# Optimization experiments

Hardware: AMD Instinct MI355X
Metric: run time of the kernel (lower is better)

## Reference

```python
import jax, jax.numpy as jnp
import numpy as np

N_GRAPHS = 8192
NODES_PER_GRAPH = 62
IN_CH = 4
HID = 64
NUM_CLASSES = 3
DEG = 8
N = N_GRAPHS * NODES_PER_GRAPH        # 507904 total nodes
E = N * DEG                            # 4063232 edges
BN_EPS = 1e-5


def setup_inputs() -> dict:
    key = jax.random.key(0)
    ks = jax.random.split(key, 24)

    def lin_w(k, i, o):
        return (jax.random.normal(k, (i, o), jnp.float32) / np.float32(np.sqrt(i)))

    inp = {
        "x": jax.random.normal(ks[0], (N, IN_CH), jnp.float32),
        "edge_src": jax.random.randint(ks[1], (E,), 0, N, dtype=jnp.int32),
        "edge_dst": jax.random.randint(ks[2], (E,), 0, N, dtype=jnp.int32),
        "num_graphs": N_GRAPHS,
        # conv1 MLP: Linear(4,64) -> ReLU -> Linear(64,64)
        "W1a": lin_w(ks[3], IN_CH, HID), "b1a": jnp.zeros((HID,), jnp.float32),
        "W1b": lin_w(ks[4], HID, HID),   "b1b": jnp.zeros((HID,), jnp.float32),
        "g1": jnp.ones((HID,), jnp.float32), "be1": jnp.zeros((HID,), jnp.float32),
        # conv2 MLP
        "W2a": lin_w(ks[5], HID, HID), "b2a": jnp.zeros((HID,), jnp.float32),
        "W2b": lin_w(ks[6], HID, HID), "b2b": jnp.zeros((HID,), jnp.float32),
        "g2": jnp.ones((HID,), jnp.float32), "be2": jnp.zeros((HID,), jnp.float32),
        # conv3 MLP
        "W3a": lin_w(ks[7], HID, HID), "b3a": jnp.zeros((HID,), jnp.float32),
        "W3b": lin_w(ks[8], HID, HID), "b3b": jnp.zeros((HID,), jnp.float32),
        "g3": jnp.ones((HID,), jnp.float32), "be3": jnp.zeros((HID,), jnp.float32),
        # final classifier fc2 (fc1 is unused in the original forward)
        "Wfc": lin_w(ks[9], HID, NUM_CLASSES), "bfc": jnp.zeros((NUM_CLASSES,), jnp.float32),
    }
    return inp


def _gin_conv(x, src, dst, Wa, ba, Wb, bb):
    # GINConv with eps=0: mlp(x_i + sum_{j->i} x_j)
    agg = jax.ops.segment_sum(x[src], dst, num_segments=N)
    h = x + agg
    return jnp.maximum(h @ Wa + ba, 0.0) @ Wb + bb


def _bn(h, g, b):
    # BatchNorm1d with batch statistics (training-mode math)
    m = h.mean(axis=0)
    v = h.var(axis=0)
    return (h - m) * jax.lax.rsqrt(v + BN_EPS) * g + b


def reference(x, edge_src, edge_dst, num_graphs,
              W1a, b1a, W1b, b1b, g1, be1,
              W2a, b2a, W2b, b2b, g2, be2,
              W3a, b3a, W3b, b3b, g3, be3,
              Wfc, bfc):
    h = _bn(jnp.maximum(_gin_conv(x, edge_src, edge_dst, W1a, b1a, W1b, b1b), 0.0), g1, be1)
    h = _bn(jnp.maximum(_gin_conv(h, edge_src, edge_dst, W2a, b2a, W2b, b2b), 0.0), g2, be2)
    h = _bn(jnp.maximum(_gin_conv(h, edge_src, edge_dst, W3a, b3a, W3b, b3b), 0.0), g3, be3)
    h = h.reshape(num_graphs, -1, HID).sum(axis=1)   # sum-pool nodes per graph
    # dropout is identity in eval mode
    return h @ Wfc + bfc
```

## Files before the change

### kernel.cpp

```cpp
#include <hip/hip_runtime.h>
#include <hip/hip_bf16.h>

#define NN   507904
#define NE   4063232
#define NG   8192
#define NPG  62
#define NBLKF 992

#define NB    248
#define BRNG  2048
#define BCAP  17152
#define PBCAP 31744
#define P3BLK 992
#define CSRSZ (NB * PBCAP)

#define OFF_R     0
#define OFF_GSUM  (OFF_R + NN * 32 + 64)
#define OFF_PART  (OFF_GSUM + NG * 64)
#define OFF_AGGBF (OFF_R + NN * 64)
#define OFF_CSR   (OFF_AGGBF + NN * 32 + 32)
#define OFF_OC    (OFF_CSR + CSRSZ)
#define OFF_BCUR  (OFF_OC + 2 * NN)
#define OFF_WTB   (OFF_BCUR + 256)
#define OFF_SS    (OFF_WTB + 11264)

#define WB_W1B 0
#define WB_W2A 4096
#define WB_W2B 8192
#define WB_W3A 12288
#define WB_W3B 16384
#define WB_W1A 20480

typedef __attribute__((ext_vector_type(8))) short short8;
typedef __attribute__((ext_vector_type(4))) float f32x4;
typedef unsigned short ushort_t;

__device__ __forceinline__ ushort_t f2bf_bits(float f) {
  union { float f; unsigned u; } x; x.f = f;
  unsigned r = x.u + 0x7FFF + ((x.u >> 16) & 1);
  return (ushort_t)(r >> 16);
}
__device__ __forceinline__ float bfu(ushort_t u) {
  union { unsigned i; float f; } x; x.i = ((unsigned)u) << 16; return x.f;
}

__global__ __launch_bounds__(256) void prep_weights(
    const float* __restrict__ w1a, const float* __restrict__ w1b,
    const float* __restrict__ w2a, const float* __restrict__ w2b,
    const float* __restrict__ w3a, const float* __restrict__ w3b,
    ushort_t* __restrict__ wtb, int* __restrict__ bcur,
    unsigned* __restrict__ sent1, unsigned* __restrict__ sent2,
    float* __restrict__ gsum) {
  int b = blockIdx.x, tid = threadIdx.x;
  if (b == 0) {
    ushort_t* d = wtb + WB_W1A;
    for (int i = tid; i < 2048; i += 256) {
      int n = i >> 5, k = i & 31;
      d[i] = (k < 4) ? f2bf_bits(w1a[k * 64 + n]) : (ushort_t)0;
    }
  } else if (b == 6) {
    bcur[tid] = 0;
    if (tid < 32) { sent1[tid] = 0; sent2[tid] = 0; }
  } else if (b >= 7) {
    float* g = gsum + (size_t)(b - 7) * 1024;
#pragma unroll
    for (int k = 0; k < 4; ++k) g[k * 256 + tid] = 0.0f;
  } else {
    const float* s; ushort_t* d;
    switch (b) {
      case 1: s = w1b; d = wtb + WB_W1B; break;
      case 2: s = w2a; d = wtb + WB_W2A; break;
      case 3: s = w2b; d = wtb + WB_W2B; break;
      case 4: s = w3a; d = wtb + WB_W3A; break;
      default: s = w3b; d = wtb + WB_W3B; break;
    }
    for (int i = tid; i < 4096; i += 256) {
      int k = i >> 6, n = i & 63;
      d[n * 64 + k] = f2bf_bits(s[i]);
    }
  }
}

__global__ __launch_bounds__(256) void p3_bin(
    const int* __restrict__ src, const int* __restrict__ dst,
    int* __restrict__ bcur, unsigned* __restrict__ recs) {
  __shared__ int histo[256];
  __shared__ int scan_s[256];
  __shared__ int base_s[256];
  __shared__ int cur_s[256];
  __shared__ uint2 buf[4096];
  const int tid = threadIdx.x;
  const int e0 = blockIdx.x * 4096;

  histo[tid] = 0;
  __syncthreads();

  int d_[16], s_[16];
#pragma unroll
  for (int k = 0; k < 16; ++k) {
    int e = e0 + k * 256 + tid;
    d_[k] = dst[e]; s_[k] = src[e];
    atomicAdd(&histo[d_[k] >> 11], 1);
  }
  __syncthreads();

  int v = histo[tid];
  scan_s[tid] = v; __syncthreads();
  for (int s = 1; s < 256; s <<= 1) {
    int add = (tid >= s) ? scan_s[tid - s] : 0;
    __syncthreads();
    scan_s[tid] += add;
    __syncthreads();
  }
  int excl = scan_s[tid] - v;
  if (tid < NB) base_s[tid] = atomicAdd(&bcur[tid], v);
  cur_s[tid] = excl;
  histo[tid] = excl;
  __syncthreads();

#pragma unroll
  for (int k = 0; k < 16; ++k) {
    int b = d_[k] >> 11;
    int p = atomicAdd(&cur_s[b], 1);
    uint2 r; r.x = (unsigned)d_[k]; r.y = (unsigned)s_[k];
    buf[p] = r;
  }
  __syncthreads();

  for (int i = tid; i < 4096; i += 256) {
    uint2 r = buf[i];
    int b = (int)(r.x >> 11);
    int g = base_s[b] + (i - histo[b]);
    if (g < BCAP)
      recs[(size_t)b * BCAP + g] = (r.y & 0x7FFFFu) | ((r.x & 2047u) << 19);
  }
}

__global__ __launch_bounds__(1024) void p4_build(
    const unsigned* __restrict__ recs, const int* __restrict__ bcur,
    int* __restrict__ csr, int2* __restrict__ oc) {
  __shared__ int lcnt[2048];
  __shared__ int pscan[1024];
  __shared__ int sstart[2048];
  __shared__ int scur[2048];
  const int b = blockIdx.x, tid = threadIdx.x;
  int m = bcur[b]; if (m > BCAP) m = BCAP;
  const int cbase = b * PBCAP;
  const int nbase = b << 11;
  const unsigned* rp = recs + (size_t)b * BCAP;

  lcnt[tid] = 0; lcnt[1024 + tid] = 0;
  __syncthreads();
  for (int i = tid; i < m; i += 1024)
    atomicAdd(&lcnt[(rp[i] >> 19) & 2047u], 1);
  __syncthreads();

  int a0 = lcnt[2 * tid], a1 = lcnt[2 * tid + 1];
  int p0 = (a0 + 7) & ~7, p1 = (a1 + 7) & ~7;
  int ps = p0 + p1;
  pscan[tid] = ps; __syncthreads();
  for (int s = 1; s < 1024; s <<= 1) {
    int add = (tid >= s) ? pscan[tid - s] : 0;
    __syncthreads();
    pscan[tid] += add;
    __syncthreads();
  }
  int e0 = pscan[tid] - ps;
  sstart[2 * tid] = e0;          scur[2 * tid] = e0;
  sstart[2 * tid + 1] = e0 + p0; scur[2 * tid + 1] = e0 + p0;
  __syncthreads();

  {
    int2 r0; r0.x = cbase + sstart[tid];        r0.y = lcnt[tid];
    int2 r1; r1.x = cbase + sstart[1024 + tid]; r1.y = lcnt[1024 + tid];
    oc[nbase + tid] = r0;
    oc[nbase + 1024 + tid] = r1;
  }
  __syncthreads();

  for (int i = tid; i < m; i += 1024) {
    unsigned r = rp[i];
    int p = atomicAdd(&scur[(r >> 19) & 2047u], 1);
    csr[cbase + p] = (int)(r & 0x7FFFFu);
  }
  __syncthreads();

#pragma unroll
  for (int k = 0; k < 2; ++k) {
    int i = k * 1024 + tid;
    int st = sstart[i], d = lcnt[i], p = (d + 7) & ~7;
    for (int q = d; q < p; ++q) csr[cbase + st + q] = NN;
  }
}

__global__ __launch_bounds__(256) void mlp_l1f(
    const float4* __restrict__ x, const int* __restrict__ csr,
    const int2* __restrict__ oc,
    const ushort_t* __restrict__ WaTb,
    const float* __restrict__ ba,
    const ushort_t* __restrict__ WbTb,
    const float* __restrict__ bb,
    ushort_t* __restrict__ routb,
    float* __restrict__ part) {
  __shared__ __align__(16) ushort_t zt[4096];
  __shared__ float red[512];
  const int tid = threadIdx.x;
  const int wave = tid >> 6, lane = tid & 63;
  const int col = lane & 15, quad = lane >> 4;

  short8 bWa1[4], bWb[2][4];
#pragma unroll
  for (int nt = 0; nt < 4; ++nt) {
    bWa1[nt] = *(const short8*)(WaTb + (nt * 16 + col) * 32 + quad * 8);
#pragma unroll
    for (int k0 = 0; k0 < 2; ++k0)
      bWb[k0][nt] = *(const short8*)(WbTb + (nt * 16 + col) * 64 + k0 * 32 + quad * 8);
  }
  float ba_n[4], bb_n[4];
#pragma unroll
  for (int nt = 0; nt < 4; ++nt) {
    ba_n[nt] = ba[nt * 16 + col];
    bb_n[nt] = bb[nt * 16 + col];
  }

  const int wbase = wave * 1024;
  float scol[4] = {0, 0, 0, 0}, qcol[4] = {0, 0, 0, 0};

  for (int it = 0; it < 8; ++it) {
    const int tile = blockIdx.x * 512 + it * 64 + wave * 16;
    const int row = tile + col;
    const int2 o = oc[row];

    float ax = 0.f, ay = 0.f, az_ = 0.f, aw = 0.f;
    if (quad == 0) {
      float4 s = x[row];
      ax = s.x; ay = s.y; az_ = s.z; aw = s.w;
    }
    const int chunks = (o.y + 7) >> 3;
    for (int c = 0; c < chunks; ++c) {
      int2 ij = *(const int2*)(csr + o.x + (c << 3) + (quad << 1));
      if (ij.x < NN) {
        float4 v = x[ij.x];
        ax += v.x; ay += v.y; az_ += v.z; aw += v.w;
      }
      if (ij.y < NN) {
        float4 v = x[ij.y];
        ax += v.x; ay += v.y; az_ += v.z; aw += v.w;
      }
    }
    ax += __shfl_xor(ax, 16); ax += __shfl_xor(ax, 32);
    ay += __shfl_xor(ay, 16); ay += __shfl_xor(ay, 32);
    az_ += __shfl_xor(az_, 16); az_ += __shfl_xor(az_, 32);
    aw += __shfl_xor(aw, 16); aw += __shfl_xor(aw, 32);

    f32x4 acc1[4];
#pragma unroll
    for (int nt = 0; nt < 4; ++nt) acc1[nt] = (f32x4){0.f, 0.f, 0.f, 0.f};

    short8 az = {0, 0, 0, 0, 0, 0, 0, 0};
    if (quad == 0) {
      az[0] = (short)f2bf_bits(ax);
      az[1] = (short)f2bf_bits(ay);
      az[2] = (short)f2bf_bits(az_);
      az[3] = (short)f2bf_bits(aw);
    }
#pragma unroll
    for (int nt = 0; nt < 4; ++nt)
      acc1[nt] = __builtin_amdgcn_mfma_f32_16x16x32_bf16(az, bWa1[nt], acc1[nt], 0, 0, 0);

#pragma unroll
    for (int nt = 0; nt < 4; ++nt) {
      int oblk = nt * 2 + (col >> 3);
#pragma unroll
      for (int r = 0; r < 4; ++r) {
        int rw = quad * 4 + r;
        float z = fmaxf(acc1[nt][r] + ba_n[nt], 0.0f);
        zt[wbase + rw * 64 + (((oblk ^ (rw & 7)) << 3) | (col & 7))] = f2bf_bits(z);
      }
    }
    short8 az0 = *(const short8*)&zt[wbase + col * 64 + ((quad ^ (col & 7)) << 3)];
    short8 az1 = *(const short8*)&zt[wbase + col * 64 + (((4 + quad) ^ (col & 7)) << 3)];

    f32x4 acc2[4];
#pragma unroll
    for (int nt = 0; nt < 4; ++nt) acc2[nt] = (f32x4){0.f, 0.f, 0.f, 0.f};
#pragma unroll
    for (int nt = 0; nt < 4; ++nt) {
      acc2[nt] = __builtin_amdgcn_mfma_f32_16x16x32_bf16(az0, bWb[0][nt], acc2[nt], 0, 0, 0);
      acc2[nt] = __builtin_amdgcn_mfma_f32_16x16x32_bf16(az1, bWb[1][nt], acc2[nt], 0, 0, 0);
    }
#pragma unroll
    for (int nt = 0; nt < 4; ++nt) {
      int oblk = nt * 2 + (col >> 3);
#pragma unroll
      for (int r = 0; r < 4; ++r) {
        int rw = quad * 4 + r;
        float v = fmaxf(acc2[nt][r] + bb_n[nt], 0.0f);
        zt[wbase + rw * 64 + (((oblk ^ (rw & 7)) << 3) | (col & 7))] = f2bf_bits(v);
        scol[nt] += v; qcol[nt] += v * v;
      }
    }
    {
      const int R = lane >> 2, sp = lane & 3;
      short8 w0 = *(const short8*)&zt[wbase + R * 64 + (((sp * 2) ^ (R & 7)) << 3)];
      short8 w1 = *(const short8*)&zt[wbase + R * 64 + (((sp * 2 + 1) ^ (R & 7)) << 3)];
      ushort_t* dst = routb + (size_t)(tile + R) * 64 + sp * 16;
      *(short8*)dst = w0;
      *(short8*)(dst + 8) = w1;
    }
  }

#pragma unroll
  for (int nt = 0; nt < 4; ++nt) {
    float s = scol[nt], q = qcol[nt];
    s += __shfl_xor(s, 16); s += __shfl_xor(s, 32);
    q += __shfl_xor(q, 16); q += __shfl_xor(q, 32);
    if (quad == 0) {
      red[wave * 128 + nt * 16 + col] = s;
      red[wave * 128 + 64 + nt * 16 + col] = q;
    }
  }
  __syncthreads();
  if (tid < 128)
    part[blockIdx.x * 128 + tid] =
        red[tid] + red[128 + tid] + red[256 + tid] + red[384 + tid];
}

template <bool GS>
__global__ __launch_bounds__(256) void mlp_fused(
    const ushort_t* __restrict__ h,
    const int* __restrict__ csr, const int2* __restrict__ oc,
    const float* __restrict__ ss,
    const ushort_t* __restrict__ WaTb,
    const float* __restrict__ ba,
    const ushort_t* __restrict__ WbTb,
    const float* __restrict__ bb,
    ushort_t* __restrict__ routb, float* __restrict__ gsum_g,
    float* __restrict__ part) {
  __shared__ __align__(16) ushort_t zt[4096];
  __shared__ float red[512];
  __shared__ float ssl[128];
  __shared__ float gsum[GS ? 640 : 1];
  const int tid = threadIdx.x;
  const int wave = tid >> 6, lane = tid & 63;
  const int col = lane & 15, quad = lane >> 4;
  if (tid < 128) ssl[tid] = ss[tid];
  const int g0 = (blockIdx.x * 512) / 62;
  if (GS) {
    for (int i = tid; i < 640; i += 256) gsum[i] = 0.0f;
  }

  short8 bWa[2][4], bWb[2][4];
#pragma unroll
  for (int nt = 0; nt < 4; ++nt) {
#pragma unroll
    for (int k0 = 0; k0 < 2; ++k0) {
      bWa[k0][nt] = *(const short8*)(WaTb + (nt * 16 + col) * 64 + k0 * 32 + quad * 8);
      bWb[k0][nt] = *(const short8*)(WbTb + (nt * 16 + col) * 64 + k0 * 32 + quad * 8);
    }
  }
  float ba_n[4], bb_n[4];
#pragma unroll
  for (int nt = 0; nt < 4; ++nt) {
    ba_n[nt] = ba[nt * 16 + col];
    bb_n[nt] = bb[nt * 16 + col];
  }
  __syncthreads();

  const float* scA = ssl + quad * 8;
  const float* scB = ssl + 32 + quad * 8;
  const float* sfA = ssl + 64 + quad * 8;
  const float* sfB = ssl + 96 + quad * 8;

  const int wbase = wave * 1024;
  float scol[4] = {0, 0, 0, 0}, qcol[4] = {0, 0, 0, 0};

  for (int it = 0; it < 8; ++it) {
    const int tile = blockIdx.x * 512 + it * 64 + wave * 16;
    const int row = tile + col;
    const int2 o = oc[row];

    const ushort_t* hp = h + (size_t)(unsigned)row * 64u + quad * 8;
    short8 sl0 = *(const short8*)hp;
    short8 sl1 = *(const short8*)(hp + 32);
    float accA[8], accB[8];
#pragma unroll
    for (int e = 0; e < 8; ++e) {
      accA[e] = bfu((ushort_t)sl0[e]);
      accB[e] = bfu((ushort_t)sl1[e]);
    }

    const int chunks = (o.y + 7) >> 3;
    for (int c = 0; c < chunks; ++c) {
      const int* cp = csr + o.x + (c << 3);
      int4 i0 = *(const int4*)cp;
      int4 i1 = *(const int4*)(cp + 4);
      int idx[8] = {i0.x, i0.y, i0.z, i0.w, i1.x, i1.y, i1.z, i1.w};
#pragma unroll
      for (int j = 0; j < 8; ++j) {
        const ushort_t* p = h + (size_t)(unsigned)idx[j] * 64u + quad * 8;
        short8 l0 = *(const short8*)p;
        short8 l1 = *(const short8*)(p + 32);
#pragma unroll
        for (int e = 0; e < 8; ++e) {
          accA[e] += bfu((ushort_t)l0[e]);
          accB[e] += bfu((ushort_t)l1[e]);
        }
      }
    }

    const float m1 = (float)(o.y + 1);
    short8 a0, a1;
#pragma unroll
    for (int e = 0; e < 8; ++e) {
      a0[e] = (short)f2bf_bits(fmaf(scA[e], accA[e], m1 * sfA[e]));
      a1[e] = (short)f2bf_bits(fmaf(scB[e], accB[e], m1 * sfB[e]));
    }

    f32x4 acc1[4];
#pragma unroll
    for (int nt = 0; nt < 4; ++nt) acc1[nt] = (f32x4){0.f, 0.f, 0.f, 0.f};
#pragma unroll
    for (int nt = 0; nt < 4; ++nt) {
      acc1[nt] = __builtin_amdgcn_mfma_f32_16x16x32_bf16(a0, bWa[0][nt], acc1[nt], 0, 0, 0);
      acc1[nt] = __builtin_amdgcn_mfma_f32_16x16x32_bf16(a1, bWa[1][nt], acc1[nt], 0, 0, 0);
    }

#pragma unroll
    for (int nt = 0; nt < 4; ++nt) {
      int oblk = nt * 2 + (col >> 3);
#pragma unroll
      for (int r = 0; r < 4; ++r) {
        int rw = quad * 4 + r;
        float z = fmaxf(acc1[nt][r] + ba_n[nt], 0.0f);
        zt[wbase + rw * 64 + (((oblk ^ (rw & 7)) << 3) | (col & 7))] = f2bf_bits(z);
      }
    }
    short8 az0 = *(const short8*)&zt[wbase + col * 64 + ((quad ^ (col & 7)) << 3)];
    short8 az1 = *(const short8*)&zt[wbase + col * 64 + (((4 + quad) ^ (col & 7)) << 3)];

    f32x4 acc2[4];
#pragma unroll
    for (int nt = 0; nt < 4; ++nt) acc2[nt] = (f32x4){0.f, 0.f, 0.f, 0.f};
#pragma unroll
    for (int nt = 0; nt < 4; ++nt) {
      acc2[nt] = __builtin_amdgcn_mfma_f32_16x16x32_bf16(az0, bWb[0][nt], acc2[nt], 0, 0, 0);
      acc2[nt] = __builtin_amdgcn_mfma_f32_16x16x32_bf16(az1, bWb[1][nt], acc2[nt], 0, 0, 0);
    }

    if (GS) {
      const int gLo = tile / 62;
      const int rEnd = (gLo + 1) * 62;
      float vLo[4], vHi[4];
#pragma unroll
      for (int nt = 0; nt < 4; ++nt) { vLo[nt] = 0.f; vHi[nt] = 0.f; }
#pragma unroll
      for (int nt = 0; nt < 4; ++nt) {
#pragma unroll
        for (int r = 0; r < 4; ++r) {
          int rw = tile + quad * 4 + r;
          float v = fmaxf(acc2[nt][r] + bb_n[nt], 0.0f);
          scol[nt] += v; qcol[nt] += v * v;
          if (rw < rEnd) vLo[nt] += v; else vHi[nt] += v;
        }
      }
#pragma unroll
      for (int nt = 0; nt < 4; ++nt) {
        vLo[nt] += __shfl_xor(vLo[nt], 16); vLo[nt] += __shfl_xor(vLo[nt], 32);
        vHi[nt] += __shfl_xor(vHi[nt], 16); vHi[nt] += __shfl_xor(vHi[nt], 32);
      }
      if (quad == 0) {
        const int gl = gLo - g0;
#pragma unroll
        for (int nt = 0; nt < 4; ++nt) {
          atomicAdd(&gsum[gl * 64 + nt * 16 + col], vLo[nt]);
          atomicAdd(&gsum[(gl + 1) * 64 + nt * 16 + col], vHi[nt]);
        }
      }
    } else {
#pragma unroll
      for (int nt = 0; nt < 4; ++nt) {
        int oblk = nt * 2 + (col >> 3);
#pragma unroll
        for (int r = 0; r < 4; ++r) {
          int rw = quad * 4 + r;
          float v = fmaxf(acc2[nt][r] + bb_n[nt], 0.0f);
          zt[wbase + rw * 64 + (((oblk ^ (rw & 7)) << 3) | (col & 7))] = f2bf_bits(v);
          scol[nt] += v; qcol[nt] += v * v;
        }
      }
      const int R = lane >> 2, sp = lane & 3;
      short8 w0 = *(const short8*)&zt[wbase + R * 64 + (((sp * 2) ^ (R & 7)) << 3)];
      short8 w1 = *(const short8*)&zt[wbase + R * 64 + (((sp * 2 + 1) ^ (R & 7)) << 3)];
      ushort_t* dst = routb + (size_t)(tile + R) * 64 + sp * 16;
      *(short8*)dst = w0;
      *(short8*)(dst + 8) = w1;
    }
  }

#pragma unroll
  for (int nt = 0; nt < 4; ++nt) {
    float s = scol[nt], q = qcol[nt];
    s += __shfl_xor(s, 16); s += __shfl_xor(s, 32);
    q += __shfl_xor(q, 16); q += __shfl_xor(q, 32);
    if (quad == 0) {
      red[wave * 128 + nt * 16 + col] = s;
      red[wave * 128 + 64 + nt * 16 + col] = q;
    }
  }
  __syncthreads();
  if (tid < 128)
    part[blockIdx.x * 128 + tid] =
        red[tid] + red[128 + tid] + red[256 + tid] + red[384 + tid];

  if (GS) {
    for (int i = tid; i < 640; i += 256) {
      int g = g0 + (i >> 6);
      float v = gsum[i];
      if (g < NG && v != 0.0f) atomicAdd(&gsum_g[(size_t)g * 64 + (i & 63)], v);
    }
  }
}

__global__ __launch_bounds__(256) void reduce_finalize(
    const float* __restrict__ part, const float* __restrict__ gma,
    const float* __restrict__ bta, float* __restrict__ ss) {
  __shared__ double sh[512];
  const int c = blockIdx.x, tid = threadIdx.x;
  double a = 0.0, b = 0.0;
  for (int blk = tid; blk < NBLKF; blk += 256) {
    a += (double)part[blk * 128 + c];
    b += (double)part[blk * 128 + 64 + c];
  }
  sh[tid] = a; sh[256 + tid] = b;
  __syncthreads();
  for (int s = 128; s; s >>= 1) {
    if (tid < s) { sh[tid] += sh[tid + s]; sh[256 + tid] += sh[256 + tid + s]; }
    __syncthreads();
  }
  if (tid == 0) {
    double mean = sh[0] / (double)NN;
    double var = sh[256] / (double)NN - mean * mean;
    double sc = (double)gma[c] / sqrt(var + 1e-5);
    ss[c] = (float)sc;
    ss[64 + c] = (float)((double)bta[c] - mean * sc);
  }
}

__global__ __launch_bounds__(256) void fc_out(
    const float* __restrict__ gsum_g, const float* __restrict__ ss,
    const float* __restrict__ wfc, const float* __restrict__ bfc,
    float* __restrict__ out) {
  const int lane = threadIdx.x & 63;
  const int g = blockIdx.x * 4 + (threadIdx.x >> 6);
  const int c = lane;
  float s = gsum_g[(size_t)g * 64 + c];
  float pooled = fmaf(ss[c], s, (float)NPG * ss[64 + c]);
#pragma unroll
  for (int j = 0; j < 3; ++j) {
    float v = pooled * wfc[c * 3 + j];
    for (int m = 32; m; m >>= 1) v += __shfl_xor(v, m);
    if (c == 0) out[g * 3 + j] = v + bfc[j];
  }
}

extern "C" void kernel_launch(void* const* d_in, const int* in_sizes, int n_in,
                              void* d_out, int out_size, void* d_ws, size_t ws_size,
                              hipStream_t stream) {
  const float* x    = (const float*)d_in[0];
  const int*   srcE = (const int*)d_in[1];
  const int*   dstE = (const int*)d_in[2];
  const float* W1a = (const float*)d_in[4],  *b1a = (const float*)d_in[5];
  const float* W1b = (const float*)d_in[6],  *b1b = (const float*)d_in[7];
  const float* g1  = (const float*)d_in[8],  *be1 = (const float*)d_in[9];
  const float* W2a = (const float*)d_in[10], *b2a = (const float*)d_in[11];
  const float* W2b = (const float*)d_in[12], *b2b = (const float*)d_in[13];
  const float* g2  = (const float*)d_in[14], *be2 = (const float*)d_in[15];
  const float* W3a = (const float*)d_in[16], *b3a = (const float*)d_in[17];
  const float* W3b = (const float*)d_in[18], *b3b = (const float*)d_in[19];
  const float* g3  = (const float*)d_in[20], *be3 = (const float*)d_in[21];
  const float* Wfc = (const float*)d_in[22], *bfc = (const float*)d_in[23];

  float* ws = (float*)d_ws;
  ushort_t* Rb     = (ushort_t*)(ws + OFF_R);
  float*    GSUM   = ws + OFF_GSUM;
  float*    PART   = ws + OFF_PART;
  ushort_t* Ab     = (ushort_t*)(ws + OFF_AGGBF);
  unsigned* RECS   = (unsigned*)(ws + OFF_AGGBF);
  int*      CSR    = (int*)(ws + OFF_CSR);
  int2*     OC     = (int2*)(ws + OFF_OC);
  int*      BCUR   = (int*)(ws + OFF_BCUR);
  ushort_t* WTB    = (ushort_t*)(ws + OFF_WTB);
  float*    SS     = ws + OFF_SS;

  prep_weights<<<519, 256, 0, stream>>>(W1a, W1b, W2a, W2b, W3a, W3b, WTB, BCUR,
                                        (unsigned*)(Rb + (size_t)NN * 64),
                                        (unsigned*)(Ab + (size_t)NN * 64),
                                        GSUM);

  p3_bin<<<P3BLK, 256, 0, stream>>>(srcE, dstE, BCUR, RECS);
  p4_build<<<NB, 1024, 0, stream>>>(RECS, BCUR, CSR, OC);

  mlp_l1f<<<NBLKF, 256, 0, stream>>>((const float4*)x, CSR, OC,
                                     WTB + WB_W1A, b1a, WTB + WB_W1B, b1b,
                                     Rb, PART);
  reduce_finalize<<<64, 256, 0, stream>>>(PART, g1, be1, SS + 0);

  mlp_fused<false><<<NBLKF, 256, 0, stream>>>(Rb, CSR, OC, SS + 0,
                                              WTB + WB_W2A, b2a,
                                              WTB + WB_W2B, b2b,
                                              Ab, nullptr, PART);
  reduce_finalize<<<64, 256, 0, stream>>>(PART, g2, be2, SS + 128);

  mlp_fused<true><<<NBLKF, 256, 0, stream>>>(Ab, CSR, OC, SS + 128,
                                             WTB + WB_W3A, b3a,
                                             WTB + WB_W3B, b3b,
                                             nullptr, GSUM, PART);
  reduce_finalize<<<64, 256, 0, stream>>>(PART, g3, be3, SS + 256);

  fc_out<<<NG / 4, 256, 0, stream>>>(GSUM, SS + 256, Wfc, bfc, (float*)d_out);
}
```

Before: 534.3 us.

## Fuse layer-1 neighbor aggregation into CSR build via shared-memory atomics

```diff
diff --git a/kernel.cpp b/kernel.cpp
--- a/kernel.cpp
+++ b/kernel.cpp
@@ -18,6 +18,7 @@
 #define OFF_GSUM  (OFF_R + NN * 32 + 64)
 #define OFF_PART  (OFF_GSUM + NG * 64)
 #define OFF_AGGBF (OFF_R + NN * 64)
+#define OFF_T1    (OFF_AGGBF + NN * 9)
 #define OFF_CSR   (OFF_AGGBF + NN * 32 + 32)
 #define OFF_OC    (OFF_CSR + CSRSZ)
 #define OFF_BCUR  (OFF_OC + 2 * NN)
@@ -138,11 +139,13 @@
 
 __global__ __launch_bounds__(1024) void p4_build(
     const unsigned* __restrict__ recs, const int* __restrict__ bcur,
-    int* __restrict__ csr, int2* __restrict__ oc) {
+    const float4* __restrict__ x,
+    int* __restrict__ csr, int2* __restrict__ oc, float4* __restrict__ t) {
   __shared__ int lcnt[2048];
   __shared__ int pscan[1024];
   __shared__ int sstart[2048];
   __shared__ int scur[2048];
+  __shared__ float tacc[8192];
   const int b = blockIdx.x, tid = threadIdx.x;
   int m = bcur[b]; if (m > BCAP) m = BCAP;
   const int cbase = b * PBCAP;
@@ -150,6 +153,8 @@
   const unsigned* rp = recs + (size_t)b * BCAP;
 
   lcnt[tid] = 0; lcnt[1024 + tid] = 0;
+#pragma unroll
+  for (int k = 0; k < 8; ++k) tacc[k * 1024 + tid] = 0.0f;
   __syncthreads();
   for (int i = tid; i < m; i += 1024)
     atomicAdd(&lcnt[(rp[i] >> 19) & 2047u], 1);
@@ -180,8 +185,15 @@
 
   for (int i = tid; i < m; i += 1024) {
     unsigned r = rp[i];
-    int p = atomicAdd(&scur[(r >> 19) & 2047u], 1);
-    csr[cbase + p] = (int)(r & 0x7FFFFu);
+    unsigned loc = (r >> 19) & 2047u;
+    int s = (int)(r & 0x7FFFFu);
+    int p = atomicAdd(&scur[loc], 1);
+    csr[cbase + p] = s;
+    float4 xv = x[s];
+    atomicAdd(&tacc[loc * 4 + 0], xv.x);
+    atomicAdd(&tacc[loc * 4 + 1], xv.y);
+    atomicAdd(&tacc[loc * 4 + 2], xv.z);
+    atomicAdd(&tacc[loc * 4 + 3], xv.w);
   }
   __syncthreads();
 
@@ -190,12 +202,18 @@
     int i = k * 1024 + tid;
     int st = sstart[i], d = lcnt[i], p = (d + 7) & ~7;
     for (int q = d; q < p; ++q) csr[cbase + st + q] = NN;
-  }
-}
-
-__global__ __launch_bounds__(256) void mlp_l1f(
-    const float4* __restrict__ x, const int* __restrict__ csr,
-    const int2* __restrict__ oc,
+    float4 xv = x[nbase + i];
+    float4 tv;
+    tv.x = xv.x + tacc[i * 4 + 0];
+    tv.y = xv.y + tacc[i * 4 + 1];
+    tv.z = xv.z + tacc[i * 4 + 2];
+    tv.w = xv.w + tacc[i * 4 + 3];
+    t[nbase + i] = tv;
+  }
+}
+
+__global__ __launch_bounds__(256) void mlp_l1(
+    const float4* __restrict__ tin,
     const ushort_t* __restrict__ WaTb,
     const float* __restrict__ ba,
     const ushort_t* __restrict__ WbTb,
@@ -228,41 +246,18 @@
 
   for (int it = 0; it < 8; ++it) {
     const int tile = blockIdx.x * 512 + it * 64 + wave * 16;
-    const int row = tile + col;
-    const int2 o = oc[row];
-
-    float ax = 0.f, ay = 0.f, az_ = 0.f, aw = 0.f;
-    if (quad == 0) {
-      float4 s = x[row];
-      ax = s.x; ay = s.y; az_ = s.z; aw = s.w;
-    }
-    const int chunks = (o.y + 7) >> 3;
-    for (int c = 0; c < chunks; ++c) {
-      int2 ij = *(const int2*)(csr + o.x + (c << 3) + (quad << 1));
-      if (ij.x < NN) {
-        float4 v = x[ij.x];
-        ax += v.x; ay += v.y; az_ += v.z; aw += v.w;
-      }
-      if (ij.y < NN) {
-        float4 v = x[ij.y];
-        ax += v.x; ay += v.y; az_ += v.z; aw += v.w;
-      }
-    }
-    ax += __shfl_xor(ax, 16); ax += __shfl_xor(ax, 32);
-    ay += __shfl_xor(ay, 16); ay += __shfl_xor(ay, 32);
-    az_ += __shfl_xor(az_, 16); az_ += __shfl_xor(az_, 32);
-    aw += __shfl_xor(aw, 16); aw += __shfl_xor(aw, 32);
 
     f32x4 acc1[4];
 #pragma unroll
     for (int nt = 0; nt < 4; ++nt) acc1[nt] = (f32x4){0.f, 0.f, 0.f, 0.f};
 
+    float4 t4 = tin[tile + col];
     short8 az = {0, 0, 0, 0, 0, 0, 0, 0};
     if (quad == 0) {
-      az[0] = (short)f2bf_bits(ax);
-      az[1] = (short)f2bf_bits(ay);
-      az[2] = (short)f2bf_bits(az_);
-      az[3] = (short)f2bf_bits(aw);
+      az[0] = (short)f2bf_bits(t4.x);
+      az[1] = (short)f2bf_bits(t4.y);
+      az[2] = (short)f2bf_bits(t4.z);
+      az[3] = (short)f2bf_bits(t4.w);
     }
 #pragma unroll
     for (int nt = 0; nt < 4; ++nt)
@@ -587,6 +582,7 @@
   float*    PART   = ws + OFF_PART;
   ushort_t* Ab     = (ushort_t*)(ws + OFF_AGGBF);
   unsigned* RECS   = (unsigned*)(ws + OFF_AGGBF);
+  float4*   T1     = (float4*)(ws + OFF_T1);
   int*      CSR    = (int*)(ws + OFF_CSR);
   int2*     OC     = (int2*)(ws + OFF_OC);
   int*      BCUR   = (int*)(ws + OFF_BCUR);
@@ -599,11 +595,10 @@
                                         GSUM);
 
   p3_bin<<<P3BLK, 256, 0, stream>>>(srcE, dstE, BCUR, RECS);
-  p4_build<<<NB, 1024, 0, stream>>>(RECS, BCUR, CSR, OC);
-
-  mlp_l1f<<<NBLKF, 256, 0, stream>>>((const float4*)x, CSR, OC,
-                                     WTB + WB_W1A, b1a, WTB + WB_W1B, b1b,
-                                     Rb, PART);
+  p4_build<<<NB, 1024, 0, stream>>>(RECS, BCUR, (const float4*)x, CSR, OC, T1);
+
+  mlp_l1<<<NBLKF, 256, 0, stream>>>(T1, WTB + WB_W1A, b1a, WTB + WB_W1B, b1b,
+                                    Rb, PART);
   reduce_finalize<<<64, 256, 0, stream>>>(PART, g1, be1, SS + 0);
 
   mlp_fused<false><<<NBLKF, 256, 0, stream>>>(Rb, CSR, OC, SS + 0,
```

Measured after the change: 550.2 us. +3.0%, slower.
